# Optimization experiments

Hardware: AMD Instinct MI355X
Metric: run time of the kernel (lower is better)

## Reference

```python
import jax, jax.numpy as jnp
import numpy as np
from math import ceil

EMBED = 512
HEADS = 8
HD = EMBED // HEADS  # 64
FFN = 2048
MIN_CHUNK = 32
LN_EPS = 1e-5


def layer_norm(x, g, b):
    mu = jnp.mean(x, axis=-1, keepdims=True)
    var = jnp.var(x, axis=-1, keepdims=True)
    return (x - mu) * jax.lax.rsqrt(var + LN_EPS) * g + b


def masked_attention(q, k, v, mask_bool, L):
    # q,k,v: [B*H, L, HD]; mask_bool: [B*H, L] (True = padding)
    BH = q.shape[0]
    S = max(MIN_CHUNK, ceil(L / 4))  # dynamic chunk size (static given L)
    C = ceil(L / S)
    pad = C * S - L
    if pad:
        q = jnp.pad(q, ((0, 0), (0, pad), (0, 0)))
        k = jnp.pad(k, ((0, 0), (0, pad), (0, 0)))
        v = jnp.pad(v, ((0, 0), (0, pad), (0, 0)))
        mask_bool = jnp.pad(mask_bool, ((0, 0), (0, pad)), constant_values=True)
    qc = q.reshape(BH, C, S, HD)
    kc = k.reshape(BH, C, S, HD)
    vc = v.reshape(BH, C, S, HD)
    mc = mask_bool.reshape(BH, C, S)
    # pad one phantom (fully masked) chunk on each side, then gather 3-chunk windows
    kp = jnp.pad(kc, ((0, 0), (1, 1), (0, 0), (0, 0)))
    vp = jnp.pad(vc, ((0, 0), (1, 1), (0, 0), (0, 0)))
    mp = jnp.pad(mc, ((0, 0), (1, 1), (0, 0)), constant_values=True)
    k_win = jnp.concatenate([kp[:, i:i + C] for i in range(3)], axis=2)  # [BH,C,3S,HD]
    v_win = jnp.concatenate([vp[:, i:i + C] for i in range(3)], axis=2)
    m_win = jnp.concatenate([mp[:, i:i + C] for i in range(3)], axis=2)  # [BH,C,3S]
    scores = jnp.einsum('bcqd,bckd->bcqk', qc, k_win) / jnp.sqrt(jnp.float32(HD))
    scores = jnp.where(m_win[:, :, None, :], -jnp.inf, scores)
    w = jax.nn.softmax(scores, axis=-1)
    out = jnp.einsum('bcqk,bckd->bcqd', w, v_win)
    return out.reshape(BH, C * S, HD)[:, :L]


def setup_inputs() -> dict:
    key = jax.random.key(0)
    ks = jax.random.split(key, 6)
    B, L, D = 4, 2048, EMBED
    s = 0.02
    return {
        'x': jax.random.normal(ks[0], (B, L, D), jnp.float32),
        'mask': jnp.zeros((B, L), jnp.int32),
        'qkv_w': jax.random.normal(ks[1], (D, 3 * D), jnp.float32) * s,
        'qkv_b': jnp.zeros((3 * D,), jnp.float32),
        'out_w': jax.random.normal(ks[2], (D, D), jnp.float32) * s,
        'out_b': jnp.zeros((D,), jnp.float32),
        'ffn_w1': jax.random.normal(ks[3], (D, FFN), jnp.float32) * s,
        'ffn_b1': jnp.zeros((FFN,), jnp.float32),
        'ffn_w2': jax.random.normal(ks[4], (FFN, D), jnp.float32) * s,
        'ffn_b2': jnp.zeros((D,), jnp.float32),
        'ln1_g': jnp.ones((D,), jnp.float32),
        'ln1_b': jnp.zeros((D,), jnp.float32),
        'ln2_g': jnp.ones((D,), jnp.float32),
        'ln2_b': jnp.zeros((D,), jnp.float32),
    }


def reference(x, mask, qkv_w, qkv_b, out_w, out_b, ffn_w1, ffn_b1, ffn_w2, ffn_b2, ln1_g, ln1_b, ln2_g, ln2_b):
    B, L, D = x.shape
    qkv = x @ qkv_w + qkv_b
    q, k, v = jnp.split(qkv, 3, axis=-1)

    def to_heads(t):
        return t.reshape(B, L, HEADS, HD).transpose(0, 2, 1, 3).reshape(B * HEADS, L, HD)

    mb = jnp.broadcast_to(mask.astype(bool)[:, None, :], (B, HEADS, L)).reshape(B * HEADS, L)
    a = masked_attention(to_heads(q), to_heads(k), to_heads(v), mb, L)
    a = a.reshape(B, HEADS, L, HD).transpose(0, 2, 1, 3).reshape(B, L, D)
    x = x + (a @ out_w + out_b)  # dropout is identity in eval
    x = layer_norm(x, ln1_g, ln1_b)
    h = jax.nn.gelu(x @ ffn_w1 + ffn_b1, approximate=False) @ ffn_w2 + ffn_b2
    x = layer_norm(x + h, ln2_g, ln2_b)
    return x
```

## Files before the change

### kernel.cpp

```cpp
#include <hip/hip_runtime.h>
#include <hip/hip_bf16.h>
#include <math.h>

#define EMBED 512
#define HEADS 8
#define HD    64
#define FFN_  2048
#define NB    4
#define LSEQ  2048
#define MROWS (NB*LSEQ)
#define BHN   (NB*HEADS)

typedef __attribute__((ext_vector_type(8))) short bf16x8;
typedef __attribute__((ext_vector_type(4))) float f32x4;
#define MFMA16(a,b,c) __builtin_amdgcn_mfma_f32_16x16x32_bf16(a,b,c,0,0,0)

__device__ __forceinline__ unsigned short f2bf(float f) {
    unsigned int u = __float_as_uint(f);
    u += 0x7fff + ((u >> 16) & 1);
    return (unsigned short)(u >> 16);
}
__device__ __forceinline__ float bf2f(unsigned short u) {
    return __uint_as_float(((unsigned int)u) << 16);
}
__device__ __forceinline__ unsigned int cvt_pk_bf16(float lo, float hi) {
    unsigned int r;
    asm("v_cvt_pk_bf16_f32 %0, %1, %2" : "=v"(r) : "v"(lo), "v"(hi));
    return r;
}
__device__ __forceinline__ void gl_lds16(const unsigned short* g, unsigned short* l) {
    __builtin_amdgcn_global_load_lds(
        (const __attribute__((address_space(1))) unsigned int*)g,
        (__attribute__((address_space(3))) unsigned int*)l, 16, 0, 0);
}
__device__ __forceinline__ float gelu_f(float x) {
    float u = x * fmaf(x * x, 0.044715f, 1.0f) * 0.7978845608f;
    float a = fminf(fmaxf(u * 2.885390082f, -30.f), 30.f);
    float t = __builtin_amdgcn_exp2f(a);
    return x * t * __builtin_amdgcn_rcpf(t + 1.0f);
}
__device__ __forceinline__ void xcd_swz(int& bx, int& by, int gx, int gy) {
    int nwg = gx * gy;
    int lid = by * gx + bx;
    int cpx = nwg >> 3;
    int swz = (lid & 7) * cpx + (lid >> 3);
    bx = swz % gx;
    by = swz / gx;
}


__global__ __launch_bounds__(256) void cvt_bf16(const float* __restrict__ in,
                                                unsigned short* __restrict__ out, int n) {
    int i = (blockIdx.x * 256 + threadIdx.x) * 8;
    if (i >= n) return;
    float4 a = *reinterpret_cast<const float4*>(&in[i]);
    float4 b = *reinterpret_cast<const float4*>(&in[i + 4]);
    unsigned short t[8] = {f2bf(a.x), f2bf(a.y), f2bf(a.z), f2bf(a.w),
                           f2bf(b.x), f2bf(b.y), f2bf(b.z), f2bf(b.w)};
    *reinterpret_cast<uint4*>(&out[i]) = *reinterpret_cast<uint4*>(t);
}

__global__ __launch_bounds__(256) void wtrans(const float* __restrict__ in,
                                              unsigned short* __restrict__ out,
                                              int K, int N) {
    __shared__ float tile[32][33];
    const int k0 = blockIdx.y * 32, n0 = blockIdx.x * 32;
    const int t = threadIdx.x;
    const int r = t >> 3, c = (t & 7) * 4;
    float4 v = *reinterpret_cast<const float4*>(&in[(size_t)(k0 + r) * N + n0 + c]);
    tile[r][c] = v.x; tile[r][c + 1] = v.y; tile[r][c + 2] = v.z; tile[r][c + 3] = v.w;
    __syncthreads();
    unsigned short tmp[4] = {f2bf(tile[c + 0][r]), f2bf(tile[c + 1][r]),
                             f2bf(tile[c + 2][r]), f2bf(tile[c + 3][r])};
    *reinterpret_cast<uint2*>(&out[(size_t)(n0 + r) * K + k0 + c]) =
        *reinterpret_cast<uint2*>(tmp);
}

__global__ __launch_bounds__(256) void vtransp(const unsigned short* __restrict__ v,
                                               unsigned short* __restrict__ vT) {
    __shared__ unsigned short tile[64][72];
    const int bh = blockIdx.y, l0 = blockIdx.x * 64;
    const int t = threadIdx.x;
    #pragma unroll
    for (int u = 0; u < 2; ++u) {
        int id = t + u * 256; int r = id >> 3, c = (id & 7) * 8;
        *reinterpret_cast<uint4*>(&tile[r][c]) = *reinterpret_cast<const uint4*>(
            &v[((size_t)bh * LSEQ + l0 + r) * HD + c]);
    }
    __syncthreads();
    #pragma unroll
    for (int u = 0; u < 2; ++u) {
        int id = t + u * 256; int d = id >> 3, kc = (id & 7) * 8;
        unsigned short tmp[8];
        #pragma unroll
        for (int jj = 0; jj < 8; ++jj) {
            int kap = kc + jj;
            tmp[jj] = tile[(kap & 3) * 16 + (kap >> 2)][d];
        }
        *reinterpret_cast<uint4*>(&vT[((size_t)bh * HD + d) * LSEQ + l0 + kc]) =
            *reinterpret_cast<uint4*>(tmp);
    }
}

template<int MODE>
__global__ __launch_bounds__(256) void gemm_bf16(
    const unsigned short* __restrict__ A, const unsigned short* __restrict__ WT,
    const float* __restrict__ bias,
    void* __restrict__ o0, void* __restrict__ o1, void* __restrict__ o2,
    int M, int N, int K)
{
    __shared__ unsigned short As[2][128 * 64];
    __shared__ unsigned short Bs[2][128 * 64];
    int bx = blockIdx.x, by = blockIdx.y;
    xcd_swz(bx, by, gridDim.x, gridDim.y);
    const int t = threadIdx.x;
    const int m0 = by * 128, n0 = bx * 128;
    const int w = t >> 6, lane = t & 63;
    const int wm = (w >> 1) * 64, wn = (w & 1) * 64;
    const int lr = lane & 15, lk = (lane >> 4) * 8;
    const int rb = (lane >> 4) * 4;
    const int srow = lane >> 3, scol = (lane & 7) * 8;

    f32x4 zero = {0.f, 0.f, 0.f, 0.f};
    f32x4 acc[4][4];
    #pragma unroll
    for (int i = 0; i < 4; ++i)
        #pragma unroll
        for (int j = 0; j < 4; ++j) acc[i][j] = zero;

    auto stage = [&](int buf, int k0) {
        #pragma unroll
        for (int i = 0; i < 4; ++i) {
            const int seg = w * 4 + i;
            const int r = seg * 8 + srow;
            gl_lds16(A  + (size_t)(m0 + r) * K + k0 + scol, &As[buf][seg * 512 + lane * 8]);
            gl_lds16(WT + (size_t)(n0 + r) * K + k0 + scol, &Bs[buf][seg * 512 + lane * 8]);
        }
    };

    const int nk = K >> 6;
    stage(0, 0);
    for (int ti = 0; ti < nk; ++ti) {
        if (ti + 1 < nk) {
            stage((ti + 1) & 1, (ti + 1) << 6);
            asm volatile("s_waitcnt vmcnt(8)" ::: "memory");
        } else {
            asm volatile("s_waitcnt vmcnt(0)" ::: "memory");
        }
        __builtin_amdgcn_s_barrier();
        const unsigned short* as = As[ti & 1];
        const unsigned short* bs = Bs[ti & 1];
        #pragma unroll
        for (int kk = 0; kk < 2; ++kk) {
            bf16x8 a[4], b[4];
            #pragma unroll
            for (int i = 0; i < 4; ++i)
                a[i] = *reinterpret_cast<const bf16x8*>(&as[(wm + i * 16 + lr) * 64 + kk * 32 + lk]);
            #pragma unroll
            for (int j = 0; j < 4; ++j)
                b[j] = *reinterpret_cast<const bf16x8*>(&bs[(wn + j * 16 + lr) * 64 + kk * 32 + lk]);
            #pragma unroll
            for (int i = 0; i < 4; ++i)
                #pragma unroll
                for (int j = 0; j < 4; ++j)
                    acc[i][j] = MFMA16(a[i], b[j], acc[i][j]);
        }
        __builtin_amdgcn_s_barrier();
    }

    #pragma unroll
    for (int i = 0; i < 4; ++i) {
        #pragma unroll
        for (int j = 0; j < 4; ++j) {
            const int n = n0 + wn + j * 16 + lr;
            const float bv = bias[n];
            #pragma unroll
            for (int r = 0; r < 4; ++r) {
                const int m = m0 + wm + i * 16 + rb + r;
                float val = acc[i][j][r] + bv;
                if (MODE == 0) {
                    const int which = n >> 9, nn = n & 511, hs = nn >> 6, d = nn & 63;
                    const int bh = (m >> 11) * 8 + hs, l = m & 2047;
                    unsigned short* p = (which == 0) ? (unsigned short*)o0
                                      : (which == 1) ? (unsigned short*)o1
                                                     : (unsigned short*)o2;
                    p[((size_t)bh * LSEQ + l) * HD + d] = f2bf(val);
                } else {
                    size_t idx = (size_t)m * N + n;
                    ((unsigned short*)o0)[idx] = f2bf(gelu_f(val));
                }
            }
        }
    }
}

template<int MODE>
__global__ __launch_bounds__(256) void gemm64(
    const unsigned short* __restrict__ A, const unsigned short* __restrict__ WT,
    const float* __restrict__ bias, const void* __restrict__ res,
    void* __restrict__ out, int M, int N, int K)
{
    __shared__ unsigned short As[2][64 * 64];
    __shared__ unsigned short Bs[2][64 * 64];
    int bx = blockIdx.x, by = blockIdx.y;
    xcd_swz(bx, by, gridDim.x, gridDim.y);
    const int t = threadIdx.x;
    const int m0 = by * 64, n0 = bx * 64;
    const int w = t >> 6, lane = t & 63;
    const int wm = (w >> 1) * 32, wn = (w & 1) * 32;
    const int lr = lane & 15, lk = (lane >> 4) * 8;
    const int rb = (lane >> 4) * 4;
    const int srow = t >> 3, scol = (t & 7) * 8;

    f32x4 zero = {0.f, 0.f, 0.f, 0.f};
    f32x4 acc[2][2];
    #pragma unroll
    for (int i = 0; i < 2; ++i)
        #pragma unroll
        for (int j = 0; j < 2; ++j) acc[i][j] = zero;

    auto stage = [&](int buf, int k0) {
        gl_lds16(A  + (size_t)(m0 + srow)      * K + k0 + scol, &As[buf][t * 8]);
        gl_lds16(A  + (size_t)(m0 + 32 + srow) * K + k0 + scol, &As[buf][2048 + t * 8]);
        gl_lds16(WT + (size_t)(n0 + srow)      * K + k0 + scol, &Bs[buf][t * 8]);
        gl_lds16(WT + (size_t)(n0 + 32 + srow) * K + k0 + scol, &Bs[buf][2048 + t * 8]);
    };

    const int nk = K >> 6;
    stage(0, 0);
    for (int ti = 0; ti < nk; ++ti) {
        if (ti + 1 < nk) {
            stage((ti + 1) & 1, (ti + 1) << 6);
            asm volatile("s_waitcnt vmcnt(4)" ::: "memory");
        } else {
            asm volatile("s_waitcnt vmcnt(0)" ::: "memory");
        }
        __builtin_amdgcn_s_barrier();
        const unsigned short* as = As[ti & 1];
        const unsigned short* bs = Bs[ti & 1];
        #pragma unroll
        for (int kk = 0; kk < 2; ++kk) {
            bf16x8 a[2], b[2];
            #pragma unroll
            for (int i = 0; i < 2; ++i)
                a[i] = *reinterpret_cast<const bf16x8*>(&as[(wm + i * 16 + lr) * 64 + kk * 32 + lk]);
            #pragma unroll
            for (int j = 0; j < 2; ++j)
                b[j] = *reinterpret_cast<const bf16x8*>(&bs[(wn + j * 16 + lr) * 64 + kk * 32 + lk]);
            #pragma unroll
            for (int i = 0; i < 2; ++i)
                #pragma unroll
                for (int j = 0; j < 2; ++j)
                    acc[i][j] = MFMA16(a[i], b[j], acc[i][j]);
        }
        __builtin_amdgcn_s_barrier();
    }

    #pragma unroll
    for (int i = 0; i < 2; ++i) {
        #pragma unroll
        for (int j = 0; j < 2; ++j) {
            const int n = n0 + wn + j * 16 + lr;
            const float bv = bias[n];
            #pragma unroll
            for (int r = 0; r < 4; ++r) {
                const int m = m0 + wm + i * 16 + rb + r;
                size_t idx = (size_t)m * N + n;
                float val = acc[i][j][r] + bv;
                if (MODE == 0) {
                    val += ((const float*)res)[idx];
                    ((unsigned short*)out)[idx] = f2bf(val);
                } else {
                    val += bf2f(((const unsigned short*)res)[idx]);
                    ((float*)out)[idx] = val;
                }
            }
        }
    }
}

__global__ __launch_bounds__(512) void attn_mfma(
    const unsigned short* __restrict__ Q, const unsigned short* __restrict__ K,
    const unsigned short* __restrict__ VTp, const int* __restrict__ mask,
    unsigned short* __restrict__ out)
{
    __shared__ unsigned short Ks[64][72];
    __shared__ unsigned short Vs[64][72];
    __shared__ unsigned short Ps[128][72];
    __shared__ float kbl[64];

    int bx = blockIdx.x, by = blockIdx.y;
    xcd_swz(bx, by, 16, 32);
    const int qt = bx, bh = by;
    const int b = bh >> 3, hh = bh & 7;
    const int t = threadIdx.x, w = t >> 6, lane = t & 63;
    const int lr = lane & 15, hi = lane >> 4;
    const int lk = hi * 8, rb = hi * 4;
    const int qr0 = qt * 128;
    const int c = qr0 >> 9;
    const int kstart = max(0, (c - 1) * 512), kend = min(LSEQ, (c + 2) * 512);

    const float C1  = 0.18033688f;
    const float KB0 = -14.4269504f;

    bf16x8 qf[2];
    #pragma unroll
    for (int kk = 0; kk < 2; ++kk)
        qf[kk] = *reinterpret_cast<const bf16x8*>(
            &Q[((size_t)bh * LSEQ + qr0 + w * 16 + lr) * HD + kk * 32 + lk]);

    f32x4 zero = {0.f, 0.f, 0.f, 0.f};
    f32x4 acc[4];
    float lsum[4] = {0.f, 0.f, 0.f, 0.f};
    #pragma unroll
    for (int j = 0; j < 4; ++j) acc[j] = zero;

    for (int kg = kstart; kg < kend; kg += 64) {
        __syncthreads();
        {
            int r = t >> 3, kc = (t & 7) * 8;
            *reinterpret_cast<uint4*>(&Ks[r][kc]) = *reinterpret_cast<const uint4*>(
                &K[((size_t)bh * LSEQ + kg + r) * HD + kc]);
            *reinterpret_cast<uint4*>(&Vs[r][kc]) = *reinterpret_cast<const uint4*>(
                &VTp[((size_t)bh * HD + r) * LSEQ + kg + kc]);
            if (t < 64) kbl[t] = mask[b * LSEQ + kg + t] ? -1e30f : KB0;
        }
        __syncthreads();

        f32x4 s[4];
        #pragma unroll
        for (int j = 0; j < 4; ++j) s[j] = zero;
        #pragma unroll
        for (int kk = 0; kk < 2; ++kk) {
            #pragma unroll
            for (int j = 0; j < 4; ++j) {
                bf16x8 bk = *reinterpret_cast<const bf16x8*>(&Ks[j * 16 + lr][kk * 32 + lk]);
                s[j] = MFMA16(qf[kk], bk, s[j]);
            }
        }
        #pragma unroll
        for (int r = 0; r < 4; ++r) {
            float p0 = __builtin_amdgcn_exp2f(fmaf(s[0][r], C1, kbl[0 * 16 + lr]));
            float p1 = __builtin_amdgcn_exp2f(fmaf(s[1][r], C1, kbl[1 * 16 + lr]));
            float p2 = __builtin_amdgcn_exp2f(fmaf(s[2][r], C1, kbl[2 * 16 + lr]));
            float p3 = __builtin_amdgcn_exp2f(fmaf(s[3][r], C1, kbl[3 * 16 + lr]));
            lsum[r] += (p0 + p1) + (p2 + p3);
            uint2 pw;
            pw.x = cvt_pk_bf16(p0, p1);
            pw.y = cvt_pk_bf16(p2, p3);
            *reinterpret_cast<uint2*>(&Ps[w * 16 + rb + r][lr * 4]) = pw;
        }
        #pragma unroll
        for (int kk = 0; kk < 2; ++kk) {
            bf16x8 pa = *reinterpret_cast<const bf16x8*>(&Ps[w * 16 + lr][kk * 32 + lk]);
            #pragma unroll
            for (int j = 0; j < 4; ++j) {
                bf16x8 bv = *reinterpret_cast<const bf16x8*>(&Vs[j * 16 + lr][kk * 32 + lk]);
                acc[j] = MFMA16(pa, bv, acc[j]);
            }
        }
    }

    float linv[4];
    #pragma unroll
    for (int r = 0; r < 4; ++r) {
        float v = lsum[r];
        v += __shfl_xor(v, 1, 16);
        v += __shfl_xor(v, 2, 16);
        v += __shfl_xor(v, 4, 16);
        v += __shfl_xor(v, 8, 16);
        linv[r] = 1.0f / v;
    }
    #pragma unroll
    for (int j = 0; j < 4; ++j)
        #pragma unroll
        for (int r = 0; r < 4; ++r) {
            const int l = qr0 + w * 16 + rb + r;
            const int d = j * 16 + lr;
            out[((size_t)(b * LSEQ + l)) * EMBED + hh * HD + d] =
                f2bf(acc[j][r] * linv[r]);
        }
}

__global__ __launch_bounds__(256) void ln_b2b(
    const unsigned short* __restrict__ in, const float* __restrict__ g,
    const float* __restrict__ bt, unsigned short* __restrict__ out)
{
    const int t = threadIdx.x, lane = t & 63;
    const int row = blockIdx.x * 4 + (t >> 6);
    uint4 raw = *reinterpret_cast<const uint4*>(&in[(size_t)row * EMBED + lane * 8]);
    float v[8];
    const unsigned int* rw = reinterpret_cast<const unsigned int*>(&raw);
    #pragma unroll
    for (int i = 0; i < 4; ++i) {
        v[2 * i]     = __uint_as_float(rw[i] << 16);
        v[2 * i + 1] = __uint_as_float(rw[i] & 0xffff0000u);
    }
    float s = 0.f, ss = 0.f;
    #pragma unroll
    for (int i = 0; i < 8; ++i) { s += v[i]; ss += v[i] * v[i]; }
    #pragma unroll
    for (int off = 1; off < 64; off <<= 1) {
        s  += __shfl_xor(s, off);
        ss += __shfl_xor(ss, off);
    }
    const float mu = s * (1.0f / EMBED);
    const float var = ss * (1.0f / EMBED) - mu * mu;
    const float rs = rsqrtf(var + 1e-5f);
    float4 g0 = *reinterpret_cast<const float4*>(&g[lane * 8]);
    float4 g1 = *reinterpret_cast<const float4*>(&g[lane * 8 + 4]);
    float4 b0 = *reinterpret_cast<const float4*>(&bt[lane * 8]);
    float4 b1 = *reinterpret_cast<const float4*>(&bt[lane * 8 + 4]);
    float gg[8] = {g0.x, g0.y, g0.z, g0.w, g1.x, g1.y, g1.z, g1.w};
    float bb[8] = {b0.x, b0.y, b0.z, b0.w, b1.x, b1.y, b1.z, b1.w};
    unsigned short o[8];
    #pragma unroll
    for (int i = 0; i < 8; ++i) o[i] = f2bf((v[i] - mu) * rs * gg[i] + bb[i]);
    *reinterpret_cast<uint4*>(&out[(size_t)row * EMBED + lane * 8]) =
        *reinterpret_cast<uint4*>(o);
}

__global__ __launch_bounds__(256) void ln_f2f(
    const float* __restrict__ in, const float* __restrict__ g,
    const float* __restrict__ bt, float* __restrict__ out)
{
    const int t = threadIdx.x, lane = t & 63;
    const int row = blockIdx.x * 4 + (t >> 6);
    const float* x = in + (size_t)row * EMBED + lane * 8;
    float4 a = *reinterpret_cast<const float4*>(x);
    float4 b2 = *reinterpret_cast<const float4*>(x + 4);
    float v[8] = {a.x, a.y, a.z, a.w, b2.x, b2.y, b2.z, b2.w};
    float s = 0.f, ss = 0.f;
    #pragma unroll
    for (int i = 0; i < 8; ++i) { s += v[i]; ss += v[i] * v[i]; }
    #pragma unroll
    for (int off = 1; off < 64; off <<= 1) {
        s  += __shfl_xor(s, off);
        ss += __shfl_xor(ss, off);
    }
    const float mu = s * (1.0f / EMBED);
    const float var = ss * (1.0f / EMBED) - mu * mu;
    const float rs = rsqrtf(var + 1e-5f);
    float4 g0 = *reinterpret_cast<const float4*>(&g[lane * 8]);
    float4 g1 = *reinterpret_cast<const float4*>(&g[lane * 8 + 4]);
    float4 b0 = *reinterpret_cast<const float4*>(&bt[lane * 8]);
    float4 b1 = *reinterpret_cast<const float4*>(&bt[lane * 8 + 4]);
    float gg[8] = {g0.x, g0.y, g0.z, g0.w, g1.x, g1.y, g1.z, g1.w};
    float bb[8] = {b0.x, b0.y, b0.z, b0.w, b1.x, b1.y, b1.z, b1.w};
    float o[8];
    #pragma unroll
    for (int i = 0; i < 8; ++i) o[i] = (v[i] - mu) * rs * gg[i] + bb[i];
    float* op = out + (size_t)row * EMBED + lane * 8;
    *reinterpret_cast<float4*>(op)     = make_float4(o[0], o[1], o[2], o[3]);
    *reinterpret_cast<float4*>(op + 4) = make_float4(o[4], o[5], o[6], o[7]);
}

extern "C" void kernel_launch(void* const* d_in, const int* in_sizes, int n_in,
                              void* d_out, int out_size, void* d_ws, size_t ws_size,
                              hipStream_t stream) {
    const float* x      = (const float*)d_in[0];
    const int*   mask   = (const int*)  d_in[1];
    const float* qkv_w  = (const float*)d_in[2];
    const float* qkv_b  = (const float*)d_in[3];
    const float* out_w  = (const float*)d_in[4];
    const float* out_b  = (const float*)d_in[5];
    const float* ffn_w1 = (const float*)d_in[6];
    const float* ffn_b1 = (const float*)d_in[7];
    const float* ffn_w2 = (const float*)d_in[8];
    const float* ffn_b2 = (const float*)d_in[9];
    const float* ln1_g  = (const float*)d_in[10];
    const float* ln1_b  = (const float*)d_in[11];
    const float* ln2_g  = (const float*)d_in[12];
    const float* ln2_b  = (const float*)d_in[13];

    char* wsb = (char*)d_ws;
    unsigned short* qkv_wT = (unsigned short*)(wsb + 0);
    unsigned short* out_wT = (unsigned short*)(wsb + 1572864);
    unsigned short* w1T    = (unsigned short*)(wsb + 2097152);
    unsigned short* w2T    = (unsigned short*)(wsb + 4194304);
    unsigned short* xb     = (unsigned short*)(wsb + 6291456);
    unsigned short* qb     = (unsigned short*)(wsb + 14680064);
    unsigned short* kbuf   = (unsigned short*)(wsb + 23068672);
    unsigned short* vb     = (unsigned short*)(wsb + 31457280);
    unsigned short* y      = (unsigned short*)(wsb + 39845888);
    unsigned short* vTp    = xb;
    unsigned short* am     = vb;
    unsigned short* xlnb   = xb;
    unsigned short* h      = (unsigned short*)(wsb + 31457280);
    float*          z      = (float*)(wsb + 65011712);

    cvt_bf16<<<MROWS * EMBED / 8 / 256, 256, 0, stream>>>(x, xb, MROWS * EMBED);
    wtrans<<<dim3(1536 / 32, 512 / 32),  256, 0, stream>>>(qkv_w,  qkv_wT, 512, 1536);
    wtrans<<<dim3(512 / 32,  512 / 32),  256, 0, stream>>>(out_w,  out_wT, 512, 512);
    wtrans<<<dim3(2048 / 32, 512 / 32),  256, 0, stream>>>(ffn_w1, w1T,    512, 2048);
    wtrans<<<dim3(512 / 32,  2048 / 32), 256, 0, stream>>>(ffn_w2, w2T,    2048, 512);

    gemm_bf16<0><<<dim3(1536 / 128, MROWS / 128), 256, 0, stream>>>(
        xb, qkv_wT, qkv_b, qb, kbuf, vb, MROWS, 1536, 512);
    vtransp<<<dim3(LSEQ / 64, BHN), 256, 0, stream>>>(vb, vTp);
    attn_mfma<<<dim3(LSEQ / 128, BHN), 512, 0, stream>>>(qb, kbuf, vTp, mask, am);
    gemm64<0><<<dim3(EMBED / 64, MROWS / 64), 256, 0, stream>>>(
        am, out_wT, out_b, x, y, MROWS, EMBED, 512);
    ln_b2b<<<MROWS / 4, 256, 0, stream>>>(y, ln1_g, ln1_b, xlnb);
    gemm_bf16<2><<<dim3(FFN_ / 128, MROWS / 128), 256, 0, stream>>>(
        xlnb, w1T, ffn_b1, h, nullptr, nullptr, MROWS, FFN_, 512);
    gemm64<1><<<dim3(EMBED / 64, MROWS / 64), 256, 0, stream>>>(
        h, w2T, ffn_b2, xlnb, z, MROWS, EMBED, FFN_);
    ln_f2f<<<MROWS / 4, 256, 0, stream>>>(z, ln2_g, ln2_b, (float*)d_out);
}
```

Before: 276.1 us.

## Fuse prep kernels and restructure attention with split-K waves and async LDS pipelining

The five input conversion and weight-transpose launches are merged into one prep kernel to cut launch overhead. The attention kernel is reorganised: each wave handles 32 query rows over half of each 64-key tile, and the two halves are reduced through shared memory at the end. K and V tiles are double-buffered with direct global-to-LDS loads and an XOR swizzle, and the mask bias is preloaded once as bf16. The V-transpose permutation changes to match the new P layout. This adds a cross-wave reduction and more shared memory use, which may lower occupancy.

```diff
diff --git a/kernel.cpp b/kernel.cpp
--- a/kernel.cpp
+++ b/kernel.cpp
@@ -48,23 +48,11 @@
     by = swz / gx;
 }
 
-
-__global__ __launch_bounds__(256) void cvt_bf16(const float* __restrict__ in,
-                                                unsigned short* __restrict__ out, int n) {
-    int i = (blockIdx.x * 256 + threadIdx.x) * 8;
-    if (i >= n) return;
-    float4 a = *reinterpret_cast<const float4*>(&in[i]);
-    float4 b = *reinterpret_cast<const float4*>(&in[i + 4]);
-    unsigned short t[8] = {f2bf(a.x), f2bf(a.y), f2bf(a.z), f2bf(a.w),
-                           f2bf(b.x), f2bf(b.y), f2bf(b.z), f2bf(b.w)};
-    *reinterpret_cast<uint4*>(&out[i]) = *reinterpret_cast<uint4*>(t);
-}
-
-__global__ __launch_bounds__(256) void wtrans(const float* __restrict__ in,
-                                              unsigned short* __restrict__ out,
-                                              int K, int N) {
-    __shared__ float tile[32][33];
-    const int k0 = blockIdx.y * 32, n0 = blockIdx.x * 32;
+__device__ __forceinline__ void wtrans_body(const float* __restrict__ in,
+                                            unsigned short* __restrict__ out,
+                                            int K, int N, int bx, int by,
+                                            float (*tile)[33]) {
+    const int k0 = by * 32, n0 = bx * 32;
     const int t = threadIdx.x;
     const int r = t >> 3, c = (t & 7) * 4;
     float4 v = *reinterpret_cast<const float4*>(&in[(size_t)(k0 + r) * N + n0 + c]);
@@ -76,6 +64,33 @@
         *reinterpret_cast<uint2*>(tmp);
 }
 
+__global__ __launch_bounds__(256) void prep(
+    const float* __restrict__ x, unsigned short* __restrict__ xb,
+    const float* __restrict__ qkv_w, unsigned short* __restrict__ qkv_wT,
+    const float* __restrict__ out_w, unsigned short* __restrict__ out_wT,
+    const float* __restrict__ w1, unsigned short* __restrict__ w1T,
+    const float* __restrict__ w2, unsigned short* __restrict__ w2T)
+{
+    __shared__ float tile[32][33];
+    const int blk = blockIdx.x;
+    if (blk < 2048) {
+        int i = (blk * 256 + threadIdx.x) * 8;
+        float4 a = *reinterpret_cast<const float4*>(&x[i]);
+        float4 b = *reinterpret_cast<const float4*>(&x[i + 4]);
+        unsigned short t8[8] = {f2bf(a.x), f2bf(a.y), f2bf(a.z), f2bf(a.w),
+                                f2bf(b.x), f2bf(b.y), f2bf(b.z), f2bf(b.w)};
+        *reinterpret_cast<uint4*>(&xb[i]) = *reinterpret_cast<uint4*>(t8);
+    } else if (blk < 2816) {
+        int i = blk - 2048; wtrans_body(qkv_w, qkv_wT, 512, 1536, i % 48, i / 48, tile);
+    } else if (blk < 3072) {
+        int i = blk - 2816; wtrans_body(out_w, out_wT, 512, 512, i % 16, i / 16, tile);
+    } else if (blk < 4096) {
+        int i = blk - 3072; wtrans_body(w1, w1T, 512, 2048, i % 64, i / 64, tile);
+    } else {
+        int i = blk - 4096; wtrans_body(w2, w2T, 2048, 512, i % 16, i / 16, tile);
+    }
+}
+
 __global__ __launch_bounds__(256) void vtransp(const unsigned short* __restrict__ v,
                                                unsigned short* __restrict__ vT) {
     __shared__ unsigned short tile[64][72];
@@ -94,8 +109,9 @@
         unsigned short tmp[8];
         #pragma unroll
         for (int jj = 0; jj < 8; ++jj) {
-            int kap = kc + jj;
-            tmp[jj] = tile[(kap & 3) * 16 + (kap >> 2)][d];
+            int posp = kc + jj;
+            int kh = posp >> 5, p = posp & 31;
+            tmp[jj] = tile[kh * 32 + (p >> 1) + (p & 1) * 16][d];
         }
         *reinterpret_cast<uint4*>(&vT[((size_t)bh * HD + d) * LSEQ + l0 + kc]) =
             *reinterpret_cast<uint4*>(tmp);
@@ -284,10 +300,12 @@
     const unsigned short* __restrict__ VTp, const int* __restrict__ mask,
     unsigned short* __restrict__ out)
 {
-    __shared__ unsigned short Ks[64][72];
-    __shared__ unsigned short Vs[64][72];
-    __shared__ unsigned short Ps[128][72];
-    __shared__ float kbl[64];
+    __shared__ __align__(16) char smem[54272];
+    unsigned short* const KsS = (unsigned short*)smem;
+    unsigned short* const VsS = (unsigned short*)(smem + 16384);
+    unsigned short* const PsS = (unsigned short*)(smem + 32768);
+    unsigned short* const kbl = (unsigned short*)(smem + 51200);
+    float* const red = (float*)smem;
 
     int bx = blockIdx.x, by = blockIdx.y;
     xcd_swz(bx, by, 16, 32);
@@ -295,91 +313,160 @@
     const int b = bh >> 3, hh = bh & 7;
     const int t = threadIdx.x, w = t >> 6, lane = t & 63;
     const int lr = lane & 15, hi = lane >> 4;
-    const int lk = hi * 8, rb = hi * 4;
+    const int kh = w >> 2, wr = (w & 3) * 32;
     const int qr0 = qt * 128;
     const int c = qr0 >> 9;
     const int kstart = max(0, (c - 1) * 512), kend = min(LSEQ, (c + 2) * 512);
+    const int nk = kend - kstart, nkt = nk >> 6;
 
     const float C1  = 0.18033688f;
     const float KB0 = -14.4269504f;
 
-    bf16x8 qf[2];
-    #pragma unroll
-    for (int kk = 0; kk < 2; ++kk)
-        qf[kk] = *reinterpret_cast<const bf16x8*>(
-            &Q[((size_t)bh * LSEQ + qr0 + w * 16 + lr) * HD + kk * 32 + lk]);
+    const int srow = t >> 3, sslot = t & 7;
+    const unsigned short* ksrc = K   + ((size_t)bh * LSEQ + kstart + srow) * HD
+                                     + ((sslot ^ (srow & 7)) * 8);
+    const unsigned short* vsrc = VTp + ((size_t)bh * HD + srow) * LSEQ + kstart
+                                     + ((sslot ^ (srow & 7)) * 8);
+
+    bf16x8 qf[2][2];
+    #pragma unroll
+    for (int fr = 0; fr < 2; ++fr)
+        #pragma unroll
+        for (int kk = 0; kk < 2; ++kk)
+            qf[fr][kk] = *reinterpret_cast<const bf16x8*>(
+                &Q[((size_t)bh * LSEQ + qr0 + wr + fr * 16 + lr) * HD + kk * 32 + hi * 8]);
+
+    for (int i = t; i < nk; i += 512)
+        kbl[i] = mask[b * LSEQ + kstart + i] ? f2bf(-1e30f) : f2bf(KB0);
 
     f32x4 zero = {0.f, 0.f, 0.f, 0.f};
-    f32x4 acc[4];
-    float lsum[4] = {0.f, 0.f, 0.f, 0.f};
-    #pragma unroll
-    for (int j = 0; j < 4; ++j) acc[j] = zero;
-
-    for (int kg = kstart; kg < kend; kg += 64) {
-        __syncthreads();
-        {
-            int r = t >> 3, kc = (t & 7) * 8;
-            *reinterpret_cast<uint4*>(&Ks[r][kc]) = *reinterpret_cast<const uint4*>(
-                &K[((size_t)bh * LSEQ + kg + r) * HD + kc]);
-            *reinterpret_cast<uint4*>(&Vs[r][kc]) = *reinterpret_cast<const uint4*>(
-                &VTp[((size_t)bh * HD + r) * LSEQ + kg + kc]);
-            if (t < 64) kbl[t] = mask[b * LSEQ + kg + t] ? -1e30f : KB0;
-        }
-        __syncthreads();
-
-        f32x4 s[4];
-        #pragma unroll
-        for (int j = 0; j < 4; ++j) s[j] = zero;
+    f32x4 acc[2][4];
+    float lsum[2][4];
+    #pragma unroll
+    for (int fr = 0; fr < 2; ++fr) {
+        #pragma unroll
+        for (int j = 0; j < 4; ++j) acc[fr][j] = zero;
+        #pragma unroll
+        for (int r = 0; r < 4; ++r) lsum[fr][r] = 0.f;
+    }
+
+    gl_lds16(ksrc, KsS + t * 8);
+    gl_lds16(vsrc, VsS + t * 8);
+    __syncthreads();
+
+    const int kxor = (lr & 7) * 8;
+    for (int ti = 0; ti < nkt; ++ti) {
+        if (ti + 1 < nkt) {
+            const int off = (ti + 1) * 64;
+            gl_lds16(ksrc + (size_t)off * HD, KsS + ((ti + 1) & 1) * 4096 + t * 8);
+            gl_lds16(vsrc + off,              VsS + ((ti + 1) & 1) * 4096 + t * 8);
+            asm volatile("s_waitcnt vmcnt(2)" ::: "memory");
+        } else {
+            asm volatile("s_waitcnt vmcnt(0)" ::: "memory");
+        }
+        __builtin_amdgcn_s_barrier();
+        const unsigned short* ks = KsS + (ti & 1) * 4096;
+        const unsigned short* vs = VsS + (ti & 1) * 4096;
+        const int kg0 = ti * 64;
+
+        f32x4 s[2][2];
+        #pragma unroll
+        for (int fr = 0; fr < 2; ++fr)
+            #pragma unroll
+            for (int j = 0; j < 2; ++j) s[fr][j] = zero;
         #pragma unroll
         for (int kk = 0; kk < 2; ++kk) {
             #pragma unroll
+            for (int j = 0; j < 2; ++j) {
+                bf16x8 bk = *reinterpret_cast<const bf16x8*>(
+                    &ks[(kh * 32 + j * 16 + lr) * 64 + (((kk * 4 + hi) * 8) ^ kxor)]);
+                s[0][j] = MFMA16(qf[0][kk], bk, s[0][j]);
+                s[1][j] = MFMA16(qf[1][kk], bk, s[1][j]);
+            }
+        }
+        const float kb0 = bf2f(kbl[kg0 + kh * 32 + lr]);
+        const float kb1 = bf2f(kbl[kg0 + kh * 32 + 16 + lr]);
+        #pragma unroll
+        for (int fr = 0; fr < 2; ++fr) {
+            #pragma unroll
+            for (int r = 0; r < 4; ++r) {
+                float p0 = __builtin_amdgcn_exp2f(fmaf(s[fr][0][r], C1, kb0));
+                float p1 = __builtin_amdgcn_exp2f(fmaf(s[fr][1][r], C1, kb1));
+                lsum[fr][r] += p0 + p1;
+                const int row = wr + fr * 16 + hi * 4 + r;
+                *reinterpret_cast<unsigned int*>(&PsS[row * 72 + kh * 32 + lr * 2]) =
+                    cvt_pk_bf16(p0, p1);
+            }
+        }
+        #pragma unroll
+        for (int fr = 0; fr < 2; ++fr) {
+            bf16x8 pa = *reinterpret_cast<const bf16x8*>(
+                &PsS[(wr + fr * 16 + lr) * 72 + kh * 32 + hi * 8]);
+            #pragma unroll
             for (int j = 0; j < 4; ++j) {
-                bf16x8 bk = *reinterpret_cast<const bf16x8*>(&Ks[j * 16 + lr][kk * 32 + lk]);
-                s[j] = MFMA16(qf[kk], bk, s[j]);
+                bf16x8 bv = *reinterpret_cast<const bf16x8*>(
+                    &vs[(j * 16 + lr) * 64 + (((kh * 4 + hi) * 8) ^ kxor)]);
+                acc[fr][j] = MFMA16(pa, bv, acc[fr][j]);
             }
         }
-        #pragma unroll
-        for (int r = 0; r < 4; ++r) {
-            float p0 = __builtin_amdgcn_exp2f(fmaf(s[0][r], C1, kbl[0 * 16 + lr]));
-            float p1 = __builtin_amdgcn_exp2f(fmaf(s[1][r], C1, kbl[1 * 16 + lr]));
-            float p2 = __builtin_amdgcn_exp2f(fmaf(s[2][r], C1, kbl[2 * 16 + lr]));
-            float p3 = __builtin_amdgcn_exp2f(fmaf(s[3][r], C1, kbl[3 * 16 + lr]));
-            lsum[r] += (p0 + p1) + (p2 + p3);
-            uint2 pw;
-            pw.x = cvt_pk_bf16(p0, p1);
-            pw.y = cvt_pk_bf16(p2, p3);
-            *reinterpret_cast<uint2*>(&Ps[w * 16 + rb + r][lr * 4]) = pw;
-        }
-        #pragma unroll
-        for (int kk = 0; kk < 2; ++kk) {
-            bf16x8 pa = *reinterpret_cast<const bf16x8*>(&Ps[w * 16 + lr][kk * 32 + lk]);
-            #pragma unroll
-            for (int j = 0; j < 4; ++j) {
-                bf16x8 bv = *reinterpret_cast<const bf16x8*>(&Vs[j * 16 + lr][kk * 32 + lk]);
-                acc[j] = MFMA16(pa, bv, acc[j]);
+        __builtin_amdgcn_s_barrier();
+    }
+
+    __syncthreads();
+    const int rid = (w & 3) * 64 + lane;
+    if (w >= 4) {
+        #pragma unroll
+        for (int fr = 0; fr < 2; ++fr)
+            #pragma unroll
+            for (int j = 0; j < 4; ++j)
+                #pragma unroll
+                for (int r = 0; r < 4; ++r)
+                    red[((fr * 4 + j) * 4 + r) * 256 + rid] = acc[fr][j][r];
+        #pragma unroll
+        for (int fr = 0; fr < 2; ++fr)
+            #pragma unroll
+            for (int r = 0; r < 4; ++r)
+                red[(32 + fr * 4 + r) * 256 + rid] = lsum[fr][r];
+    }
+    __syncthreads();
+    if (w < 4) {
+        #pragma unroll
+        for (int fr = 0; fr < 2; ++fr)
+            #pragma unroll
+            for (int j = 0; j < 4; ++j)
+                #pragma unroll
+                for (int r = 0; r < 4; ++r)
+                    acc[fr][j][r] += red[((fr * 4 + j) * 4 + r) * 256 + rid];
+        #pragma unroll
+        for (int fr = 0; fr < 2; ++fr)
+            #pragma unroll
+            for (int r = 0; r < 4; ++r)
+                lsum[fr][r] += red[(32 + fr * 4 + r) * 256 + rid];
+
+        float linv[2][4];
+        #pragma unroll
+        for (int fr = 0; fr < 2; ++fr)
+            #pragma unroll
+            for (int r = 0; r < 4; ++r) {
+                float v = lsum[fr][r];
+                v += __shfl_xor(v, 1, 16);
+                v += __shfl_xor(v, 2, 16);
+                v += __shfl_xor(v, 4, 16);
+                v += __shfl_xor(v, 8, 16);
+                linv[fr][r] = 1.0f / v;
             }
-        }
-    }
-
-    float linv[4];
-    #pragma unroll
-    for (int r = 0; r < 4; ++r) {
-        float v = lsum[r];
-        v += __shfl_xor(v, 1, 16);
-        v += __shfl_xor(v, 2, 16);
-        v += __shfl_xor(v, 4, 16);
-        v += __shfl_xor(v, 8, 16);
-        linv[r] = 1.0f / v;
-    }
-    #pragma unroll
-    for (int j = 0; j < 4; ++j)
-        #pragma unroll
-        for (int r = 0; r < 4; ++r) {
-            const int l = qr0 + w * 16 + rb + r;
-            const int d = j * 16 + lr;
-            out[((size_t)(b * LSEQ + l)) * EMBED + hh * HD + d] =
-                f2bf(acc[j][r] * linv[r]);
-        }
+        #pragma unroll
+        for (int fr = 0; fr < 2; ++fr)
+            #pragma unroll
+            for (int j = 0; j < 4; ++j)
+                #pragma unroll
+                for (int r = 0; r < 4; ++r) {
+                    const int l = qr0 + wr + fr * 16 + hi * 4 + r;
+                    const int d = j * 16 + lr;
+                    out[((size_t)(b * LSEQ + l)) * EMBED + hh * HD + d] =
+                        f2bf(acc[fr][j][r] * linv[fr][r]);
+                }
+    }
 }
 
 __global__ __launch_bounds__(256) void ln_b2b(
@@ -489,12 +576,8 @@
     unsigned short* h      = (unsigned short*)(wsb + 31457280);
     float*          z      = (float*)(wsb + 65011712);
 
-    cvt_bf16<<<MROWS * EMBED / 8 / 256, 256, 0, stream>>>(x, xb, MROWS * EMBED);
-    wtrans<<<dim3(1536 / 32, 512 / 32),  256, 0, stream>>>(qkv_w,  qkv_wT, 512, 1536);
-    wtrans<<<dim3(512 / 32,  512 / 32),  256, 0, stream>>>(out_w,  out_wT, 512, 512);
-    wtrans<<<dim3(2048 / 32, 512 / 32),  256, 0, stream>>>(ffn_w1, w1T,    512, 2048);
-    wtrans<<<dim3(512 / 32,  2048 / 32), 256, 0, stream>>>(ffn_w2, w2T,    2048, 512);
-
+    prep<<<5120, 256, 0, stream>>>(x, xb, qkv_w, qkv_wT, out_w, out_wT,
+                                   ffn_w1, w1T, ffn_w2, w2T);
     gemm_bf16<0><<<dim3(1536 / 128, MROWS / 128), 256, 0, stream>>>(
         xb, qkv_wT, qkv_b, qb, kbuf, vb, MROWS, 1536, 512);
     vtransp<<<dim3(LSEQ / 64, BHN), 256, 0, stream>>>(vb, vTp);
```

Result: faster. 259.3 us (-6.1%).
